# Kernel optimization log

Measured on AMD Instinct MI355X. Metric: run time of the kernel, lower is better.

Reference implementation:

```python
import jax, jax.numpy as jnp
import numpy as np

_EPS = 1e-8  # cosine-similarity clamp, matching F.cosine_similarity
_MAX_NODES = 50000


def _sig(x):
    return 1.0 / (1.0 + np.exp(-x))


def _build_structure(seqs, emb, comp_l, comp_r, cb, max_nodes=_MAX_NODES):
    """Host-side faithful replay of Banyan.compose()'s sequential greedy
    agglomerative merge. Returns the (data-dependent) merge schedule so the
    differentiable part can be replayed in jax. The similarity computation uses
    detached node values in the original, so the structure is a constant wrt
    differentiation. Dropout is run in eval mode (identity)."""
    E = emb.shape[1]
    sl, sr = _sig(comp_l), _sig(comp_r)  # (4,)
    uniq = np.unique(seqs)
    lookup = np.zeros(int(uniq.max()) + 1, dtype=np.int64)
    lookup[uniq] = np.arange(len(uniq))
    lookup[-1] = -1  # batch-max token is padding
    index = lookup[seqs]
    leaves = uniq[:-1]
    n_c = np.zeros((max_nodes, E), dtype=np.float32)
    n_c[: len(leaves)] = emb[leaves]
    t_c = np.full((max_nodes, 3), -1, dtype=np.int64)
    c_c = np.full((max_nodes, 2), -1, dtype=np.int64)
    md = int(index.max())
    B = index.shape[0]
    rows = np.arange(B)
    steps = []
    while index.shape[1] != 1:
        valid = index != -1  # -1 entries are always trailing
        W = index.shape[1]
        sims = np.zeros((B, W, E), dtype=np.float32)
        sims[valid] = n_c[index[valid]]
        a, b = sims[:, :-1], sims[:, 1:]
        na = np.maximum(np.linalg.norm(a, axis=2), _EPS)
        nb = np.maximum(np.linalg.norm(b, axis=2), _EPS)
        cos = (a * b).sum(2) / (na * nb)
        cos[~valid[:, 1:]] = -np.inf  # pairs whose right slot is empty
        max_sim = cos.argmax(1)  # (B,)
        retrieval = np.stack([max_sim, max_sim + 1], axis=1)  # (B, 2)
        completion = ~np.all(index[:, 1:] == -1, axis=1)
        r_c = retrieval[completion].reshape(-1)
        idx_c = index[completion]
        if idx_c.size:
            rt = np.repeat(np.arange(idx_c.shape[0]), 2)
            src = idx_c[rt, r_c].reshape(-1, 2)
            keep_src = ~((src[:, None, :] == c_c[None, :, :]).all(2)).any(1)
            src = np.unique(src[keep_src], axis=0)
            if src.size:
                k = src.shape[0]
                dst = md + 1 + np.arange(k)
                md = int(dst.max())
                l = n_c[src[:, 0]].reshape(k, 4, 4)
                r = n_c[src[:, 1]].reshape(k, 4, 4)
                n_c[dst] = (l * sl + r * sr + cb).reshape(k, E)
                c_c[dst] = src
                steps.append((src.copy(), dst.copy()))
                L, R = r_c[::2], r_c[1::2]
                l_t = np.concatenate([L, L - 1, R])
                r_n = R + 1
                r_n = np.where(r_n > idx_c.max(), -1, r_n)
                r_t = np.concatenate([R, L, r_n])
                t = np.concatenate([l_t, r_t]).reshape(-1, 3)
                t = np.unique(t, axis=0)
                keep_t = ~((t[:, None, :] == t_c[None, :, :]).all(2)).any(1)
                t = t[keep_t]
                adds = int((t_c != -1).all(1).sum())
                t_c[adds : adds + t.shape[0]] = t
        keep = np.ones(index.shape, dtype=bool)
        keep[rows[completion], max_sim[completion]] = False
        if (~completion).any():
            keep[~completion, -1] = False
        index = index[keep].reshape(B, -1)
    targets = t_c[(t_c != -1).all(1)]
    return leaves, steps, md, targets


def _replay(embedding, comp_l, comp_r, cb, leaves, steps, md, targets):
    """Differentiable replay of the recorded merge schedule + loss."""
    E = embedding.shape[1]
    sl = jax.nn.sigmoid(comp_l)
    sr = jax.nn.sigmoid(comp_r)

    def comp(l, r):  # LCCompose with 4 channels of width 4 (E = 16)
        return (l.reshape(-1, 4, 4) * sl + r.reshape(-1, 4, 4) * sr + cb).reshape(-1, E)

    n_c = jnp.zeros((md + 1, E), embedding.dtype)
    n_c = n_c.at[: leaves.shape[0]].set(embedding[leaves])
    for src, dst in steps:  # inherently sequential merge schedule
        n_c = n_c.at[dst].set(comp(n_c[src[:, 0]], n_c[src[:, 1]]))
    lefts = n_c[targets[:, 1]]
    rights = n_c[targets[:, 2]]
    logits = comp(lefts, rights) @ n_c.T  # [T, N], K=16 -> memory bound
    logp = jax.nn.log_softmax(logits, axis=-1)
    lbl = jnp.asarray(targets[:, 0])
    return -jnp.take_along_axis(logp, lbl[:, None], axis=1).mean()


def setup_inputs() -> dict:
    key = jax.random.key(0)
    ks = jax.random.split(key, 5)
    B, S, V, E = 48, 160, 32000, 16
    seqs = jax.random.randint(ks[0], (B, S), 0, V - 1)
    lens = jax.random.randint(ks[1], (B,), S // 2, S)  # at least 1 pad per row
    seqs = jnp.where(jnp.arange(S)[None, :] < lens[:, None], seqs, V - 1)
    embedding = jax.random.normal(ks[2], (V, E), jnp.float32)
    comp_l = jax.random.uniform(ks[3], (4,), jnp.float32, 0.6, 0.9)
    comp_r = jax.random.uniform(ks[4], (4,), jnp.float32, 0.6, 0.9)
    cb = jnp.zeros((4,), jnp.float32)
    return {"seqs": seqs, "embedding": embedding, "comp_l": comp_l, "comp_r": comp_r, "cb": cb}


def reference(seqs, embedding, comp_l, comp_r, cb):
    leaves, steps, md, targets = _build_structure(
        np.asarray(seqs), np.asarray(embedding), np.asarray(comp_l),
        np.asarray(comp_r), np.asarray(cb))
    return _replay(embedding, comp_l, comp_r, cb, leaves, steps, md, targets)
```

## Files before the change

### kernel.cpp

```cpp
#include <hip/hip_runtime.h>
#include <math.h>
#include <limits.h>

#define NT 1024
#define BB 48
#define SS 160
#define VV 32000
#define PADTOK 31999
#define EE 16
#define CAP 20000
#define NWRD 640
#define PHN 32768
#define TBW (1 << 19)

__device__ int      g_pres[32768];
__device__ int      g_rank[32768];
__device__ float    g_nc[CAP][EE];
__device__ float    g_nrm[CAP];
__device__ unsigned g_ph[PHN];
__device__ unsigned g_tbm[TBW];
__device__ unsigned g_tck[CAP];
__device__ int      g_tg[CAP][3];
__device__ float    g_lo[CAP];
__device__ int      g_T, g_N;
__device__ float    g_sl[4], g_sr[4], g_cb[4];

__device__ __forceinline__ unsigned vload(const unsigned* p) {
    return *(const volatile unsigned*)p;
}

__device__ __forceinline__ float np_sum16(const float* p) {
    float r0 = __fadd_rn(p[0], p[8]);
    float r1 = __fadd_rn(p[1], p[9]);
    float r2 = __fadd_rn(p[2], p[10]);
    float r3 = __fadd_rn(p[3], p[11]);
    float r4 = __fadd_rn(p[4], p[12]);
    float r5 = __fadd_rn(p[5], p[13]);
    float r6 = __fadd_rn(p[6], p[14]);
    float r7 = __fadd_rn(p[7], p[15]);
    float a = __fadd_rn(__fadd_rn(r0, r1), __fadd_rn(r2, r3));
    float b = __fadd_rn(__fadd_rn(r4, r5), __fadd_rn(r6, r7));
    return __fadd_rn(a, b);
}

__device__ __forceinline__ int key_valid(unsigned k) {
    return (((k >> 16) & 255u) != 0u) && (((k >> 8) & 255u) != 0u) && ((k & 255u) != 0u);
}

__global__ __launch_bounds__(256)
void init_kernel()
{
    int i = blockIdx.x * 256 + threadIdx.x;
    if (i < TBW)   g_tbm[i] = 0u;
    if (i < PHN)   g_ph[i] = 0xFFFFFFFFu;
    if (i < 32768) g_pres[i] = 0;
    if (i < CAP)   g_tck[i] = 0u;
}

__global__ __launch_bounds__(NT)
void build_kernel(const int* __restrict__ seqs, const float* __restrict__ emb,
                  const float* __restrict__ comp_l, const float* __restrict__ comp_r,
                  const float* __restrict__ cbp)
{
    const int tid  = threadIdx.x;
    const int lane = tid & 63;
    const int wv   = tid >> 6;

    __shared__ short    s_idx[BB][SS];
    __shared__ float    s_cos[BB][SS];
    __shared__ int      s_nv[BB], s_ms[BB], s_comp[BB], s_rowmax[BB];
    __shared__ unsigned s_pkey[BB];
    __shared__ int      s_L[BB], s_R[BB], s_found[BB];
    __shared__ unsigned s_skey[BB], s_ssorted[BB];
    __shared__ int      s_cA[BB], s_cB[BB], s_dst[BB];
    __shared__ unsigned s_tkey[2 * BB], s_tsorted[2 * BB], s_stk[2 * BB];
    __shared__ float    s_newcos[BB];
    __shared__ unsigned s_tvb[NWRD];
    __shared__ int s_ncand, s_kcnt, s_mx, s_adds;
    __shared__ int s_md, s_hwm, s_nleaves;
    __shared__ int s_scan[NT / 64];
    __shared__ float s_sl4[4], s_sr4[4], s_cb4[4];

    if (tid < NWRD) s_tvb[tid] = 0u;
    for (int i = tid; i < BB * SS; i += NT) g_pres[seqs[i]] = 1;
    __syncthreads();
    int base = tid * 32;
    int c = 0;
    for (int k = 0; k < 32; ++k) { int v = base + k; if (v < VV) c += g_pres[v]; }
    int incl = c;
    for (int off = 1; off < 64; off <<= 1) {
        int t = __shfl_up(incl, off);
        if (lane >= off) incl += t;
    }
    if (lane == 63) s_scan[wv] = incl;
    __syncthreads();
    if (tid == 0) {
        int run = 0;
        for (int w = 0; w < NT / 64; ++w) { int t = s_scan[w]; s_scan[w] = run; run += t; }
        s_nleaves = run - 1;
        s_md = run - 2;
        s_hwm = 0;
    }
    __syncthreads();
    {
        int run = s_scan[wv] + incl - c;
        for (int k = 0; k < 32; ++k) {
            int v = base + k;
            if (v < VV && g_pres[v]) g_rank[v] = run++;
        }
    }
    __syncthreads();
    for (int v = tid; v < VV; v += NT) {
        if (g_pres[v] && v != PADTOK) {
            int r = g_rank[v];
            #pragma unroll
            for (int e = 0; e < EE; ++e) g_nc[r][e] = emb[v * EE + e];
        }
    }
    if (tid < 4) {
        float sl = 1.0f / (1.0f + expf(-comp_l[tid]));
        float sr = 1.0f / (1.0f + expf(-comp_r[tid]));
        s_sl4[tid] = sl; s_sr4[tid] = sr; s_cb4[tid] = cbp[tid];
        g_sl[tid] = sl;  g_sr[tid] = sr;  g_cb[tid] = cbp[tid];
    }
    for (int i = tid; i < BB * SS; i += NT) {
        int tok = seqs[i];
        s_idx[i / SS][i % SS] = (short)((tok == PADTOK) ? -1 : g_rank[tok]);
    }
    __syncthreads();
    const int nleaves = s_nleaves;
    for (int l = tid; l < nleaves; l += NT) {
        float p[EE];
        #pragma unroll
        for (int e = 0; e < EE; ++e) { float x = g_nc[l][e]; p[e] = __fmul_rn(x, x); }
        g_nrm[l] = fmaxf(__fsqrt_rn(np_sum16(p)), 1e-8f);
    }
    if (tid < BB) {
        int cnt = 0;
        for (int p = 0; p < SS; ++p) cnt += (s_idx[tid][p] >= 0);
        s_nv[tid] = cnt;
    }
    __syncthreads();
    for (int i = tid; i < BB * (SS - 1); i += NT) {
        int r = i / (SS - 1), p = i % (SS - 1);
        if (p < s_nv[r] - 1) {
            int a = s_idx[r][p], b = s_idx[r][p + 1];
            const float* pa = g_nc[a];
            const float* pb = g_nc[b];
            float pr[EE];
            #pragma unroll
            for (int e = 0; e < EE; ++e) pr[e] = __fmul_rn(pa[e], pb[e]);
            s_cos[r][p] = __fdiv_rn(np_sum16(pr), __fmul_rn(g_nrm[a], g_nrm[b]));
        }
    }
    __syncthreads();

    for (int it = 0; it < SS - 1; ++it) {
        const int W = SS - it;

        for (int row = wv; row < BB; row += 16) {
            int nv = s_nv[row];
            int npairs = nv - 1;
            float best = -INFINITY; int bidx = INT_MAX;
            for (int p = lane; p < npairs; p += 64) {
                float cv = s_cos[row][p];
                if (cv > best) { best = cv; bidx = p; }
            }
            int rmax = INT_MIN;
            for (int p = lane; p < W; p += 64) { int v = (int)s_idx[row][p]; if (v > rmax) rmax = v; }
            for (int off = 32; off >= 1; off >>= 1) {
                float ob = __shfl_down(best, off);
                int   oi = __shfl_down(bidx, off);
                int   om = __shfl_down(rmax, off);
                if (ob > best || (ob == best && oi < bidx)) { best = ob; bidx = oi; }
                if (om > rmax) rmax = om;
            }
            if (lane == 0) {
                s_ms[row] = (bidx == INT_MAX) ? 0 : bidx;
                s_comp[row] = (nv > 1) ? 1 : 0;
                s_rowmax[row] = rmax;
            }
        }
        if (tid == 0) s_adds = 0;
        __syncthreads();

        if (wv == 0) {
            int flag = (lane < BB) ? s_comp[lane] : 0;
            unsigned long long m = __ballot(flag);
            int rm = flag ? s_rowmax[lane] : INT_MIN;
            if (flag) {
                int pos = __popcll(m & ((1ULL << lane) - 1ULL));
                int ms = s_ms[lane];
                int a = s_idx[lane][ms], b = s_idx[lane][ms + 1];
                s_pkey[pos] = ((unsigned)a << 16) | (unsigned)b;
                s_L[pos] = ms; s_R[pos] = ms + 1;
            }
            for (int off = 32; off >= 1; off >>= 1) { int o = __shfl_down(rm, off); if (o > rm) rm = o; }
            if (lane == 0) { s_ncand = __popcll(m); s_mx = rm; }
        } else if (wv <= 3) {
            int loc = 0;
            for (int w = tid - 64; w < NWRD; w += 192) loc += __popc(s_tvb[w]);
            for (int off = 32; off >= 1; off >>= 1) loc += __shfl_down(loc, off);
            if (lane == 0 && loc) atomicAdd(&s_adds, loc);
        } else {
            int i = tid - 256;
            int row = i >> 4, e = i & 15;
            if (s_comp[row] && s_ms[row] >= 1) {
                int a = (int)s_idx[row][s_ms[row] - 1];
                int b = (int)s_idx[row][s_ms[row] + 1];
                float p = __fmul_rn(g_nc[a][e], g_nc[b][e]);
                p = __fadd_rn(p, __shfl_xor(p, 8, 16));
                p = __fadd_rn(p, __shfl_xor(p, 1, 16));
                p = __fadd_rn(p, __shfl_xor(p, 2, 16));
                p = __fadd_rn(p, __shfl_xor(p, 4, 16));
                if (e == 0) s_newcos[row] = __fdiv_rn(p, __fmul_rn(g_nrm[a], g_nrm[b]));
            }
        }
        __syncthreads();

        const int ncand = s_ncand;
        if (wv == 0) {
            if (lane < ncand) {
                unsigned k = s_pkey[lane];
                unsigned h = (k * 2654435761u) >> 17;
                int found = 0;
                while (true) {
                    unsigned v = vload(&g_ph[h]);
                    if (v == k) { found = 1; break; }
                    if (v == 0xFFFFFFFFu) break;
                    h = (h + 1) & (PHN - 1);
                }
                s_found[lane] = found;
            }
        } else if (wv <= 2) {
            int j = tid - 64;
            if (j < 2 * ncand) {
                int comps[3];
                #pragma unroll
                for (int cc = 0; cc < 3; ++cc) {
                    int i = 3 * j + cc;
                    int seg = i / ncand, q = i - seg * ncand;
                    int v;
                    switch (seg) {
                        case 0: v = s_L[q]; break;
                        case 1: v = s_L[q] - 1; break;
                        case 2: v = s_R[q]; break;
                        case 3: v = s_R[q]; break;
                        case 4: v = s_L[q]; break;
                        default: { int rn = s_R[q] + 1; v = (rn > s_mx) ? -1 : rn; } break;
                    }
                    comps[cc] = v;
                }
                s_tkey[j] = ((unsigned)(comps[0] + 1) << 16) | ((unsigned)(comps[1] + 1) << 8)
                          | (unsigned)(comps[2] + 1);
            }
        }
        __syncthreads();

        if (wv == 0) {
            int flag = (lane < ncand) ? (s_found[lane] == 0) : 0;
            unsigned long long m = __ballot(flag);
            if (flag) {
                int pos = __popcll(m & ((1ULL << lane) - 1ULL));
                s_skey[pos] = s_pkey[lane];
            }
            int kn = __popcll(m);
            if (lane < kn) {
                unsigned ki = s_skey[lane];
                int rk = 0;
                for (int j = 0; j < kn; ++j) {
                    unsigned kj = s_skey[j];
                    if (kj < ki || (kj == ki && j < lane)) rk++;
                }
                s_ssorted[rk] = ki;
            }
            int mdold = s_md;
            int f2 = 0;
            if (lane < kn) {
                unsigned k = s_ssorted[lane];
                f2 = (lane == 0) || (k != s_ssorted[lane - 1]);
            }
            unsigned long long m2 = __ballot(f2);
            int kcnt = __popcll(m2);
            if (f2) {
                int pos = __popcll(m2 & ((1ULL << lane) - 1ULL));
                unsigned k = s_ssorted[lane];
                s_cA[pos] = (int)(k >> 16);
                s_cB[pos] = (int)(k & 0xFFFFu);
                s_dst[pos] = mdold + 1 + pos;
                unsigned h = (k * 2654435761u) >> 17;
                while (true) {
                    unsigned prev = atomicCAS(&g_ph[h], 0xFFFFFFFFu, k);
                    if (prev == 0xFFFFFFFFu) break;
                    h = (h + 1) & (PHN - 1);
                }
            }
            if (lane == 0) { s_kcnt = kcnt; s_md = mdold + kcnt; }
        } else if (wv <= 2) {
            int j = tid - 64;
            int mt0 = 2 * ncand;
            if (j < mt0) {
                unsigned ki = s_tkey[j];
                int rk = 0;
                for (int jj = 0; jj < mt0; ++jj) {
                    unsigned kj = s_tkey[jj];
                    if (kj < ki || (kj == ki && jj < j)) rk++;
                }
                s_tsorted[rk] = ki;
            }
        }
        __syncthreads();

        const int kcnt = s_kcnt;
        if (wv == 0) {
            if (kcnt > 0) {
                int mt0 = 2 * ncand;
                int cnt = 0;
                #pragma unroll
                for (int chunk = 0; chunk < 2; ++chunk) {
                    int e = chunk * 64 + lane;
                    int flag = 0;
                    if (e < mt0) {
                        unsigned k = s_tsorted[e];
                        flag = (e == 0) || (k != s_tsorted[e - 1]);
                    }
                    unsigned long long m = __ballot(flag);
                    if (flag) {
                        int pos = cnt + __popcll(m & ((1ULL << lane) - 1ULL));
                        s_stk[pos] = s_tsorted[e];
                    }
                    cnt += __popcll(m);
                }
                const int mt = cnt;
                int f0 = 0, f1 = 0;
                {
                    int j = lane;
                    if (j < mt) { unsigned k = s_stk[j]; f0 = (k == 0u) || ((vload(&g_tbm[k >> 5]) >> (k & 31)) & 1u); }
                }
                {
                    int j = 64 + lane;
                    if (j < mt) { unsigned k = s_stk[j]; f1 = (k == 0u) || ((vload(&g_tbm[k >> 5]) >> (k & 31)) & 1u); }
                }
                int adds = s_adds;
                int cnt2 = 0;
                #pragma unroll
                for (int chunk = 0; chunk < 2; ++chunk) {
                    int j = chunk * 64 + lane;
                    int f = chunk ? f1 : f0;
                    int flag = (j < mt) && !f;
                    unsigned long long m = __ballot(flag);
                    if (flag) {
                        int pos = adds + cnt2 + __popcll(m & ((1ULL << lane) - 1ULL));
                        unsigned k = s_stk[j];
                        unsigned old = g_tck[pos];
                        if (old) atomicAnd(&g_tbm[old >> 5], ~(1u << (old & 31)));
                        atomicOr(&g_tbm[k >> 5], 1u << (k & 31));
                        g_tck[pos] = k;
                        int w = pos >> 5; unsigned bm = 1u << (pos & 31);
                        atomicAnd(&s_tvb[w], ~bm);
                        if (key_valid(k)) atomicOr(&s_tvb[w], bm);
                    }
                    cnt2 += __popcll(m);
                }
                if (lane == 0) { int e2 = adds + cnt2; if (e2 > s_hwm) s_hwm = e2; }
            }
        } else if (wv <= 12) {
            for (int sub = 0; sub < 4; ++sub) {
                int row = (wv - 1) * 4 + sub;
                if (s_comp[row]) {
                    int ms = s_ms[row];
                    for (int p = ms + lane; p <= W - 2; p += 64) {
                        short v = s_idx[row][p + 1];
                        float cv = s_cos[row][p + 1];
                        s_idx[row][p] = v;
                        s_cos[row][p] = cv;
                    }
                    if (lane == 0) {
                        s_nv[row] -= 1;
                        if (ms >= 1) s_cos[row][ms - 1] = s_newcos[row];
                    }
                }
            }
        } else {
            for (int i = tid - 832; i < kcnt * EE; i += 192) {
                int j = i >> 4, e = i & 15;
                float lv = g_nc[s_cA[j]][e], rv = g_nc[s_cB[j]][e];
                g_nc[s_dst[j]][e] = lv * s_sl4[e & 3] + rv * s_sr4[e & 3] + s_cb4[e & 3];
            }
        }
        __syncthreads();
    }

    {
        int hw = s_hwm;
        int per = (hw + NT - 1) / NT;
        int b2 = tid * per;
        int cnt = 0;
        for (int k = 0; k < per; ++k) {
            int e = b2 + k;
            if (e < hw && key_valid(g_tck[e])) cnt++;
        }
        int incl2 = cnt;
        for (int off = 1; off < 64; off <<= 1) {
            int t = __shfl_up(incl2, off);
            if (lane >= off) incl2 += t;
        }
        if (lane == 63) s_scan[wv] = incl2;
        __syncthreads();
        if (tid == 0) {
            int run = 0;
            for (int w = 0; w < NT / 64; ++w) { int t = s_scan[w]; s_scan[w] = run; run += t; }
            g_T = run;
            g_N = s_md + 1;
        }
        __syncthreads();
        int off2 = s_scan[wv] + incl2 - cnt;
        for (int k = 0; k < per; ++k) {
            int e = b2 + k;
            if (e < hw) {
                unsigned kk = g_tck[e];
                if (key_valid(kk)) {
                    g_tg[off2][0] = (int)((kk >> 16) & 255u) - 1;
                    g_tg[off2][1] = (int)((kk >> 8) & 255u) - 1;
                    g_tg[off2][2] = (int)(kk & 255u) - 1;
                    off2++;
                }
            }
        }
    }
}

__global__ __launch_bounds__(256)
void loss_kernel()
{
    __shared__ float s_u[EE];
    __shared__ float s_m[256], s_s[256];
    __shared__ float s_xlab;
    const int tid = threadIdx.x;
    const int T = g_T, N = g_N;
    for (int ti = blockIdx.x; ti < T; ti += gridDim.x) {
        int lab = g_tg[ti][0], l = g_tg[ti][1], r = g_tg[ti][2];
        if (tid < EE)
            s_u[tid] = g_nc[l][tid] * g_sl[tid & 3] + g_nc[r][tid] * g_sr[tid & 3] + g_cb[tid & 3];
        __syncthreads();
        float u[EE];
        #pragma unroll
        for (int e = 0; e < EE; ++e) u[e] = s_u[e];
        float m = -INFINITY, s = 0.0f;
        for (int j = tid; j < N; j += 256) {
            const float* pj = g_nc[j];
            float x = 0.f;
            #pragma unroll
            for (int e = 0; e < EE; ++e) x += u[e] * pj[e];
            if (x > m) { s = s * expf(m - x) + 1.0f; m = x; }
            else s += expf(x - m);
            if (j == lab) s_xlab = x;
        }
        s_m[tid] = m; s_s[tid] = s;
        __syncthreads();
        for (int st = 128; st >= 1; st >>= 1) {
            if (tid < st) {
                float m1 = s_m[tid], s1 = s_s[tid];
                float m2 = s_m[tid + st], s2 = s_s[tid + st];
                if (m2 == -INFINITY) {  }
                else if (m2 > m1) { s1 = s1 * expf(m1 - m2) + s2; m1 = m2; }
                else { s1 = s1 + s2 * expf(m2 - m1); }
                s_m[tid] = m1; s_s[tid] = s1;
            }
            __syncthreads();
        }
        if (tid == 0) g_lo[ti] = s_m[0] + logf(s_s[0]) - s_xlab;
        __syncthreads();
    }
}

__global__ __launch_bounds__(256)
void finish_kernel(float* __restrict__ out)
{
    __shared__ float s_p[256];
    const int tid = threadIdx.x;
    const int T = g_T;
    float acc = 0.f;
    for (int i = tid; i < T; i += 256) acc += g_lo[i];
    s_p[tid] = acc;
    __syncthreads();
    for (int st = 128; st >= 1; st >>= 1) {
        if (tid < st) s_p[tid] += s_p[tid + st];
        __syncthreads();
    }
    if (tid == 0) out[0] = (T > 0) ? (s_p[0] / (float)T) : 0.0f;
}

extern "C" void kernel_launch(void* const* d_in, const int* in_sizes, int n_in,
                              void* d_out, int out_size, void* d_ws, size_t ws_size,
                              hipStream_t stream) {
    const int*   seqs = (const int*)d_in[0];
    const float* emb  = (const float*)d_in[1];
    const float* cl   = (const float*)d_in[2];
    const float* cr   = (const float*)d_in[3];
    const float* cb   = (const float*)d_in[4];
    float* out = (float*)d_out;
    init_kernel<<<dim3(2048), dim3(256), 0, stream>>>();
    build_kernel<<<dim3(1), dim3(NT), 0, stream>>>(seqs, emb, cl, cr, cb);
    loss_kernel<<<dim3(2048), dim3(256), 0, stream>>>();
    finish_kernel<<<dim3(1), dim3(256), 0, stream>>>(out);
}
```

Before: 1.614 ms.

## Split monolithic build into per-row merge, bookkeeping, compose, and tiled loss kernels

Replaces the single-block 1024-thread build kernel with a pipeline of kernels. Leaf copy and norms run grid-wide, and each row's greedy merge trajectory is computed independently by one 64-thread block. A single-wave bookkeeping kernel then replays the cross-row dedup and target generation from those trajectories, and composed node vectors are computed in a separate parallel kernel. The loss kernel is retiled to handle 8 targets per block with wave-shuffle reductions and fast exp/log intrinsics. This trades more launches and the approximate __expf/__logf for removing the serial per-iteration block-wide synchronisation.

```diff
diff --git a/kernel.cpp b/kernel.cpp
--- a/kernel.cpp
+++ b/kernel.cpp
@@ -2,14 +2,12 @@
 #include <math.h>
 #include <limits.h>
 
-#define NT 1024
 #define BB 48
 #define SS 160
 #define VV 32000
 #define PADTOK 31999
 #define EE 16
 #define CAP 20000
-#define NWRD 640
 #define PHN 32768
 #define TBW (1 << 19)
 
@@ -20,9 +18,12 @@
 __device__ unsigned g_ph[PHN];
 __device__ unsigned g_tbm[TBW];
 __device__ unsigned g_tck[CAP];
+__device__ unsigned long long g_traj[(SS - 1) * BB];
+__device__ int      g_steps[BB];
+__device__ unsigned long long g_new[CAP];
 __device__ int      g_tg[CAP][3];
 __device__ float    g_lo[CAP];
-__device__ int      g_T, g_N;
+__device__ int      g_T, g_N, g_nl, g_md0, g_hwm, g_mdfin, g_ncnt;
 __device__ float    g_sl[4], g_sr[4], g_cb[4];
 
 __device__ __forceinline__ unsigned vload(const unsigned* p) {
@@ -47,6 +48,29 @@
     return (((k >> 16) & 255u) != 0u) && (((k >> 8) & 255u) != 0u) && ((k & 255u) != 0u);
 }
 
+__device__ __forceinline__ unsigned make_tkey(int j, int ncand, int mx,
+                                              const int* sL, const int* sR) {
+    int comps[3];
+    #pragma unroll
+    for (int cc = 0; cc < 3; ++cc) {
+        int i = 3 * j + cc;
+        int seg = 0;
+        while (i >= ncand) { i -= ncand; ++seg; }
+        int v;
+        switch (seg) {
+            case 0: v = sL[i]; break;
+            case 1: v = sL[i] - 1; break;
+            case 2: v = sR[i]; break;
+            case 3: v = sR[i]; break;
+            case 4: v = sL[i]; break;
+            default: { int rn = sR[i] + 1; v = (rn > mx) ? -1 : rn; } break;
+        }
+        comps[cc] = v;
+    }
+    return ((unsigned)(comps[0] + 1) << 16) | ((unsigned)(comps[1] + 1) << 8)
+         | (unsigned)(comps[2] + 1);
+}
+
 __global__ __launch_bounds__(256)
 void init_kernel()
 {
@@ -57,35 +81,15 @@
     if (i < CAP)   g_tck[i] = 0u;
 }
 
-__global__ __launch_bounds__(NT)
-void build_kernel(const int* __restrict__ seqs, const float* __restrict__ emb,
-                  const float* __restrict__ comp_l, const float* __restrict__ comp_r,
-                  const float* __restrict__ cbp)
-{
-    const int tid  = threadIdx.x;
-    const int lane = tid & 63;
-    const int wv   = tid >> 6;
-
-    __shared__ short    s_idx[BB][SS];
-    __shared__ float    s_cos[BB][SS];
-    __shared__ int      s_nv[BB], s_ms[BB], s_comp[BB], s_rowmax[BB];
-    __shared__ unsigned s_pkey[BB];
-    __shared__ int      s_L[BB], s_R[BB], s_found[BB];
-    __shared__ unsigned s_skey[BB], s_ssorted[BB];
-    __shared__ int      s_cA[BB], s_cB[BB], s_dst[BB];
-    __shared__ unsigned s_tkey[2 * BB], s_tsorted[2 * BB], s_stk[2 * BB];
-    __shared__ float    s_newcos[BB];
-    __shared__ unsigned s_tvb[NWRD];
-    __shared__ int s_ncand, s_kcnt, s_mx, s_adds;
-    __shared__ int s_md, s_hwm, s_nleaves;
-    __shared__ int s_scan[NT / 64];
-    __shared__ float s_sl4[4], s_sr4[4], s_cb4[4];
-
-    if (tid < NWRD) s_tvb[tid] = 0u;
-    for (int i = tid; i < BB * SS; i += NT) g_pres[seqs[i]] = 1;
-    __syncthreads();
-    int base = tid * 32;
-    int c = 0;
+__global__ __launch_bounds__(1024)
+void rank_kernel(const int* __restrict__ seqs, const float* __restrict__ comp_l,
+                 const float* __restrict__ comp_r, const float* __restrict__ cbp)
+{
+    const int tid = threadIdx.x, lane = tid & 63, wv = tid >> 6;
+    __shared__ int s_scan[16];
+    for (int i = tid; i < BB * SS; i += 1024) g_pres[seqs[i]] = 1;
+    __syncthreads();
+    int base = tid * 32, c = 0;
     for (int k = 0; k < 32; ++k) { int v = base + k; if (v < VV) c += g_pres[v]; }
     int incl = c;
     for (int off = 1; off < 64; off <<= 1) {
@@ -96,380 +100,424 @@
     __syncthreads();
     if (tid == 0) {
         int run = 0;
-        for (int w = 0; w < NT / 64; ++w) { int t = s_scan[w]; s_scan[w] = run; run += t; }
-        s_nleaves = run - 1;
-        s_md = run - 2;
-        s_hwm = 0;
-    }
-    __syncthreads();
-    {
-        int run = s_scan[wv] + incl - c;
-        for (int k = 0; k < 32; ++k) {
-            int v = base + k;
-            if (v < VV && g_pres[v]) g_rank[v] = run++;
-        }
-    }
-    __syncthreads();
-    for (int v = tid; v < VV; v += NT) {
-        if (g_pres[v] && v != PADTOK) {
-            int r = g_rank[v];
-            #pragma unroll
-            for (int e = 0; e < EE; ++e) g_nc[r][e] = emb[v * EE + e];
-        }
+        for (int w = 0; w < 16; ++w) { int t = s_scan[w]; s_scan[w] = run; run += t; }
+        g_nl = run - 1;
+        g_md0 = run - 2;
+    }
+    __syncthreads();
+    int run = s_scan[wv] + incl - c;
+    for (int k = 0; k < 32; ++k) {
+        int v = base + k;
+        if (v < VV && g_pres[v]) g_rank[v] = run++;
     }
     if (tid < 4) {
         float sl = 1.0f / (1.0f + expf(-comp_l[tid]));
         float sr = 1.0f / (1.0f + expf(-comp_r[tid]));
-        s_sl4[tid] = sl; s_sr4[tid] = sr; s_cb4[tid] = cbp[tid];
-        g_sl[tid] = sl;  g_sr[tid] = sr;  g_cb[tid] = cbp[tid];
-    }
-    for (int i = tid; i < BB * SS; i += NT) {
-        int tok = seqs[i];
-        s_idx[i / SS][i % SS] = (short)((tok == PADTOK) ? -1 : g_rank[tok]);
-    }
-    __syncthreads();
-    const int nleaves = s_nleaves;
-    for (int l = tid; l < nleaves; l += NT) {
-        float p[EE];
-        #pragma unroll
-        for (int e = 0; e < EE; ++e) { float x = g_nc[l][e]; p[e] = __fmul_rn(x, x); }
-        g_nrm[l] = fmaxf(__fsqrt_rn(np_sum16(p)), 1e-8f);
-    }
-    if (tid < BB) {
+        g_sl[tid] = sl; g_sr[tid] = sr; g_cb[tid] = cbp[tid];
+    }
+}
+
+__global__ __launch_bounds__(256)
+void leaf_kernel(const float* __restrict__ emb)
+{
+    int v = blockIdx.x * 256 + threadIdx.x;
+    int stride = gridDim.x * 256;
+    for (; v < VV; v += stride) {
+        if (g_pres[v] && v != PADTOK) {
+            int r = g_rank[v];
+            float p[EE];
+            #pragma unroll
+            for (int e = 0; e < EE; ++e) {
+                float x = emb[v * EE + e];
+                g_nc[r][e] = x;
+                p[e] = __fmul_rn(x, x);
+            }
+            g_nrm[r] = fmaxf(__fsqrt_rn(np_sum16(p)), 1e-8f);
+        }
+    }
+}
+
+__global__ __launch_bounds__(64)
+void rowsim_kernel(const int* __restrict__ seqs)
+{
+    const int row = blockIdx.x;
+    const int lane = threadIdx.x;
+    __shared__ float s_vec[SS][17];
+    __shared__ float s_nrmp[SS];
+    __shared__ float s_cos[SS];
+    __shared__ int   s_id[SS];
+    __shared__ int   s_map[SS];
+    __shared__ int   s_nv0;
+
+    for (int p = lane; p < SS; p += 64) {
+        int tok = seqs[row * SS + p];
+        s_id[p] = (tok == PADTOK) ? -1 : g_rank[tok];
+        s_map[p] = p;
+    }
+    __syncthreads();
+    if (lane == 0) {
         int cnt = 0;
-        for (int p = 0; p < SS; ++p) cnt += (s_idx[tid][p] >= 0);
-        s_nv[tid] = cnt;
-    }
-    __syncthreads();
-    for (int i = tid; i < BB * (SS - 1); i += NT) {
-        int r = i / (SS - 1), p = i % (SS - 1);
-        if (p < s_nv[r] - 1) {
-            int a = s_idx[r][p], b = s_idx[r][p + 1];
-            const float* pa = g_nc[a];
-            const float* pb = g_nc[b];
-            float pr[EE];
+        for (int p = 0; p < SS; ++p) cnt += (s_id[p] >= 0);
+        s_nv0 = cnt;
+    }
+    __syncthreads();
+    const int nv0 = s_nv0;
+    #pragma unroll 4
+    for (int i = lane; i < nv0 * 4; i += 64) {
+        int p = i >> 2, q = i & 3;
+        const float4 v = ((const float4*)g_nc[s_id[p]])[q];
+        s_vec[p][q * 4 + 0] = v.x; s_vec[p][q * 4 + 1] = v.y;
+        s_vec[p][q * 4 + 2] = v.z; s_vec[p][q * 4 + 3] = v.w;
+    }
+    for (int p = lane; p < nv0; p += 64) s_nrmp[p] = g_nrm[s_id[p]];
+    __syncthreads();
+    for (int p = lane; p < nv0 - 1; p += 64) {
+        float pr[EE];
+        #pragma unroll
+        for (int e = 0; e < EE; ++e) pr[e] = __fmul_rn(s_vec[p][e], s_vec[p + 1][e]);
+        s_cos[p] = __fdiv_rn(np_sum16(pr), __fmul_rn(s_nrmp[p], s_nrmp[p + 1]));
+    }
+    __syncthreads();
+
+    int nv = nv0;
+    for (int st = 0; nv > 1; ++st, --nv) {
+        float best = -INFINITY; int bidx = INT_MAX; int rmax = INT_MIN;
+        for (int p = lane; p < nv; p += 64) {
+            int v = s_id[p];
+            if (v > rmax) rmax = v;
+            if (p < nv - 1) {
+                float cv = s_cos[p];
+                if (cv > best) { best = cv; bidx = p; }
+            }
+        }
+        #pragma unroll
+        for (int off = 32; off >= 1; off >>= 1) {
+            float ob = __shfl_xor(best, off);
+            int   oi = __shfl_xor(bidx, off);
+            int   om = __shfl_xor(rmax, off);
+            if (ob > best || (ob == best && oi < bidx)) { best = ob; bidx = oi; }
+            if (om > rmax) rmax = om;
+        }
+        const int ms = bidx;
+        if (lane == 0) {
+            unsigned long long a = (unsigned)s_id[ms];
+            unsigned long long b = (unsigned)s_id[ms + 1];
+            g_traj[st * BB + row] = (a << 48) | (b << 32)
+                                  | ((unsigned long long)(unsigned)ms << 16)
+                                  | (unsigned long long)(unsigned)rmax;
+        }
+        float ncv = 0.f;
+        if (ms >= 1 && lane < 16) {
+            int m1 = s_map[ms - 1], m2 = s_map[ms + 1];
+            float pp = __fmul_rn(s_vec[m1][lane], s_vec[m2][lane]);
+            pp = __fadd_rn(pp, __shfl_xor(pp, 8, 16));
+            pp = __fadd_rn(pp, __shfl_xor(pp, 1, 16));
+            pp = __fadd_rn(pp, __shfl_xor(pp, 2, 16));
+            pp = __fadd_rn(pp, __shfl_xor(pp, 4, 16));
+            ncv = __fdiv_rn(pp, __fmul_rn(s_nrmp[m1], s_nrmp[m2]));
+        }
+        __syncthreads();
+        int iv[3], mv[3]; float cv[3];
+        #pragma unroll
+        for (int k = 0; k < 3; ++k) {
+            int p = ms + lane + k * 64;
+            if (p < nv - 1) { iv[k] = s_id[p + 1]; mv[k] = s_map[p + 1]; cv[k] = s_cos[p + 1]; }
+        }
+        __syncthreads();
+        #pragma unroll
+        for (int k = 0; k < 3; ++k) {
+            int p = ms + lane + k * 64;
+            if (p < nv - 1) { s_id[p] = iv[k]; s_map[p] = mv[k]; s_cos[p] = cv[k]; }
+        }
+        if (ms >= 1 && lane == 0) s_cos[ms - 1] = ncv;
+        __syncthreads();
+    }
+    if (lane == 0) g_steps[row] = nv0 - 1;
+}
+
+__global__ __launch_bounds__(64)
+void book_kernel()
+{
+    const int lane = threadIdx.x;
+    __shared__ unsigned s_pk[64], s_ps[64];
+    __shared__ int s_Ld[64], s_Rd[64];
+    __shared__ unsigned s_tk[96], s_ts[96], s_stk[96];
+
+    const int steps = (lane < BB) ? g_steps[lane] : 0;
+    int md = g_md0;
+    int validcnt = 0, hwm = 0, ncnt = 0;
+
+    unsigned long long tr = (0 < steps) ? g_traj[lane] : 0ULL;
+    for (int it = 0; it < SS - 1; ++it) {
+        unsigned long long trn = ((it + 1) < steps) ? g_traj[(it + 1) * BB + lane] : 0ULL;
+        const int active = (it < steps) ? 1 : 0;
+        unsigned long long am = __ballot(active);
+        const int ncand = __popcll(am);
+        if (ncand > 0) {
+            const int adds = validcnt;
+            int a  = (int)(tr >> 48);
+            int b  = (int)((tr >> 32) & 0xFFFFULL);
+            int ms = (int)((tr >> 16) & 0xFFFFULL);
+            int mx = active ? (int)(tr & 0xFFFFULL) : INT_MIN;
             #pragma unroll
-            for (int e = 0; e < EE; ++e) pr[e] = __fmul_rn(pa[e], pb[e]);
-            s_cos[r][p] = __fdiv_rn(np_sum16(pr), __fmul_rn(g_nrm[a], g_nrm[b]));
-        }
-    }
-    __syncthreads();
-
-    for (int it = 0; it < SS - 1; ++it) {
-        const int W = SS - it;
-
-        for (int row = wv; row < BB; row += 16) {
-            int nv = s_nv[row];
-            int npairs = nv - 1;
-            float best = -INFINITY; int bidx = INT_MAX;
-            for (int p = lane; p < npairs; p += 64) {
-                float cv = s_cos[row][p];
-                if (cv > best) { best = cv; bidx = p; }
-            }
-            int rmax = INT_MIN;
-            for (int p = lane; p < W; p += 64) { int v = (int)s_idx[row][p]; if (v > rmax) rmax = v; }
             for (int off = 32; off >= 1; off >>= 1) {
-                float ob = __shfl_down(best, off);
-                int   oi = __shfl_down(bidx, off);
-                int   om = __shfl_down(rmax, off);
-                if (ob > best || (ob == best && oi < bidx)) { best = ob; bidx = oi; }
-                if (om > rmax) rmax = om;
-            }
-            if (lane == 0) {
-                s_ms[row] = (bidx == INT_MAX) ? 0 : bidx;
-                s_comp[row] = (nv > 1) ? 1 : 0;
-                s_rowmax[row] = rmax;
-            }
-        }
-        if (tid == 0) s_adds = 0;
-        __syncthreads();
-
-        if (wv == 0) {
-            int flag = (lane < BB) ? s_comp[lane] : 0;
-            unsigned long long m = __ballot(flag);
-            int rm = flag ? s_rowmax[lane] : INT_MIN;
-            if (flag) {
-                int pos = __popcll(m & ((1ULL << lane) - 1ULL));
-                int ms = s_ms[lane];
-                int a = s_idx[lane][ms], b = s_idx[lane][ms + 1];
-                s_pkey[pos] = ((unsigned)a << 16) | (unsigned)b;
-                s_L[pos] = ms; s_R[pos] = ms + 1;
-            }
-            for (int off = 32; off >= 1; off >>= 1) { int o = __shfl_down(rm, off); if (o > rm) rm = o; }
-            if (lane == 0) { s_ncand = __popcll(m); s_mx = rm; }
-        } else if (wv <= 3) {
-            int loc = 0;
-            for (int w = tid - 64; w < NWRD; w += 192) loc += __popc(s_tvb[w]);
-            for (int off = 32; off >= 1; off >>= 1) loc += __shfl_down(loc, off);
-            if (lane == 0 && loc) atomicAdd(&s_adds, loc);
-        } else {
-            int i = tid - 256;
-            int row = i >> 4, e = i & 15;
-            if (s_comp[row] && s_ms[row] >= 1) {
-                int a = (int)s_idx[row][s_ms[row] - 1];
-                int b = (int)s_idx[row][s_ms[row] + 1];
-                float p = __fmul_rn(g_nc[a][e], g_nc[b][e]);
-                p = __fadd_rn(p, __shfl_xor(p, 8, 16));
-                p = __fadd_rn(p, __shfl_xor(p, 1, 16));
-                p = __fadd_rn(p, __shfl_xor(p, 2, 16));
-                p = __fadd_rn(p, __shfl_xor(p, 4, 16));
-                if (e == 0) s_newcos[row] = __fdiv_rn(p, __fmul_rn(g_nrm[a], g_nrm[b]));
-            }
-        }
-        __syncthreads();
-
-        const int ncand = s_ncand;
-        if (wv == 0) {
+                int o = __shfl_xor(mx, off); if (o > mx) mx = o;
+            }
+            int cpos = __popcll(am & ((1ULL << lane) - 1ULL));
+            if (active) {
+                s_pk[cpos] = ((unsigned)a << 16) | (unsigned)b;
+                s_Ld[cpos] = ms; s_Rd[cpos] = ms + 1;
+            }
+            __syncthreads();
+            unsigned ki = (lane < ncand) ? s_pk[lane] : 0xFFFFFFFFu;
+            int rk = 0;
+            for (int j = 0; j < ncand; ++j) {
+                unsigned kj = s_pk[j];
+                if (kj < ki || (kj == ki && j < lane)) ++rk;
+            }
+            if (lane < ncand) s_ps[rk] = ki;
+            const int mt0 = 2 * ncand;
+            const int j1 = 64 + lane;
+            unsigned tk0 = 0xFFFFFFFFu, tk1 = 0xFFFFFFFFu;
+            if (lane < mt0) { tk0 = make_tkey(lane, ncand, mx, s_Ld, s_Rd); s_tk[lane] = tk0; }
+            if (j1 < mt0)   { tk1 = make_tkey(j1, ncand, mx, s_Ld, s_Rd);   s_tk[j1] = tk1; }
+            __syncthreads();
+            int r0 = 0, r1 = 0;
+            for (int j = 0; j < mt0; ++j) {
+                unsigned kj = s_tk[j];
+                if (kj < tk0 || (kj == tk0 && j < lane)) ++r0;
+                if (kj < tk1 || (kj == tk1 && j < j1)) ++r1;
+            }
+            if (lane < mt0) s_ts[r0] = tk0;
+            if (j1 < mt0)   s_ts[r1] = tk1;
+            __syncthreads();
+            unsigned k0 = s_ts[lane];
+            int fl0 = (lane < mt0) && (lane == 0 || k0 != s_ts[lane - 1]);
+            unsigned long long m0 = __ballot(fl0);
+            if (fl0) s_stk[__popcll(m0 & ((1ULL << lane) - 1ULL))] = k0;
+            int c0d = __popcll(m0);
+            unsigned k1 = (j1 < 96) ? s_ts[j1] : 0u;
+            int fl1 = (j1 < mt0) && (k1 != s_ts[j1 - 1]);
+            unsigned long long m1 = __ballot(fl1);
+            if (fl1) s_stk[c0d + __popcll(m1 & ((1ULL << lane) - 1ULL))] = k1;
+            const int mt = c0d + __popcll(m1);
+            __syncthreads();
+
+            unsigned psk = (lane < ncand) ? s_ps[lane] : 0u;
+            int pfound = 0;
             if (lane < ncand) {
-                unsigned k = s_pkey[lane];
-                unsigned h = (k * 2654435761u) >> 17;
-                int found = 0;
+                unsigned h = (psk * 2654435761u) >> 17;
                 while (true) {
                     unsigned v = vload(&g_ph[h]);
-                    if (v == k) { found = 1; break; }
+                    if (v == psk) { pfound = 1; break; }
                     if (v == 0xFFFFFFFFu) break;
                     h = (h + 1) & (PHN - 1);
                 }
-                s_found[lane] = found;
-            }
-        } else if (wv <= 2) {
-            int j = tid - 64;
-            if (j < 2 * ncand) {
-                int comps[3];
-                #pragma unroll
-                for (int cc = 0; cc < 3; ++cc) {
-                    int i = 3 * j + cc;
-                    int seg = i / ncand, q = i - seg * ncand;
-                    int v;
-                    switch (seg) {
-                        case 0: v = s_L[q]; break;
-                        case 1: v = s_L[q] - 1; break;
-                        case 2: v = s_R[q]; break;
-                        case 3: v = s_R[q]; break;
-                        case 4: v = s_L[q]; break;
-                        default: { int rn = s_R[q] + 1; v = (rn > s_mx) ? -1 : rn; } break;
-                    }
-                    comps[cc] = v;
-                }
-                s_tkey[j] = ((unsigned)(comps[0] + 1) << 16) | ((unsigned)(comps[1] + 1) << 8)
-                          | (unsigned)(comps[2] + 1);
-            }
-        }
-        __syncthreads();
-
-        if (wv == 0) {
-            int flag = (lane < ncand) ? (s_found[lane] == 0) : 0;
-            unsigned long long m = __ballot(flag);
-            if (flag) {
-                int pos = __popcll(m & ((1ULL << lane) - 1ULL));
-                s_skey[pos] = s_pkey[lane];
-            }
-            int kn = __popcll(m);
-            if (lane < kn) {
-                unsigned ki = s_skey[lane];
-                int rk = 0;
-                for (int j = 0; j < kn; ++j) {
-                    unsigned kj = s_skey[j];
-                    if (kj < ki || (kj == ki && j < lane)) rk++;
-                }
-                s_ssorted[rk] = ki;
-            }
-            int mdold = s_md;
-            int f2 = 0;
-            if (lane < kn) {
-                unsigned k = s_ssorted[lane];
-                f2 = (lane == 0) || (k != s_ssorted[lane - 1]);
-            }
-            unsigned long long m2 = __ballot(f2);
-            int kcnt = __popcll(m2);
-            if (f2) {
-                int pos = __popcll(m2 & ((1ULL << lane) - 1ULL));
-                unsigned k = s_ssorted[lane];
-                s_cA[pos] = (int)(k >> 16);
-                s_cB[pos] = (int)(k & 0xFFFFu);
-                s_dst[pos] = mdold + 1 + pos;
-                unsigned h = (k * 2654435761u) >> 17;
+            }
+            unsigned stk0 = (lane < mt) ? s_stk[lane] : 0u;
+            unsigned stk1 = (64 + lane < mt) ? s_stk[64 + lane] : 0u;
+            int tf0 = 1, tf1 = 1;
+            if (lane < mt)
+                tf0 = (stk0 == 0u) || ((vload(&g_tbm[stk0 >> 5]) >> (stk0 & 31)) & 1u);
+            if (64 + lane < mt)
+                tf1 = (stk1 == 0u) || ((vload(&g_tbm[stk1 >> 5]) >> (stk1 & 31)) & 1u);
+            unsigned old0 = vload(&g_tck[adds + lane]);
+            unsigned old1 = (lane < 32) ? vload(&g_tck[adds + 64 + lane]) : 0u;
+
+            int keptp = (lane < ncand) && !pfound;
+            int flp = keptp && (lane == 0 || s_ps[lane - 1] != psk);
+            unsigned long long mp = __ballot(flp);
+            int kcnt = __popcll(mp);
+            if (flp) {
+                int p3 = __popcll(mp & ((1ULL << lane) - 1ULL));
+                int dst = md + 1 + p3;
+                unsigned a2 = psk >> 16, b2 = psk & 0xFFFFu;
+                g_new[ncnt + p3] = ((unsigned long long)a2 << 42)
+                                 | ((unsigned long long)b2 << 21)
+                                 | (unsigned long long)(unsigned)dst;
+                unsigned h = (psk * 2654435761u) >> 17;
                 while (true) {
-                    unsigned prev = atomicCAS(&g_ph[h], 0xFFFFFFFFu, k);
+                    unsigned prev = atomicCAS(&g_ph[h], 0xFFFFFFFFu, psk);
                     if (prev == 0xFFFFFFFFu) break;
                     h = (h + 1) & (PHN - 1);
                 }
             }
-            if (lane == 0) { s_kcnt = kcnt; s_md = mdold + kcnt; }
-        } else if (wv <= 2) {
-            int j = tid - 64;
-            int mt0 = 2 * ncand;
-            if (j < mt0) {
-                unsigned ki = s_tkey[j];
-                int rk = 0;
-                for (int jj = 0; jj < mt0; ++jj) {
-                    unsigned kj = s_tkey[jj];
-                    if (kj < ki || (kj == ki && jj < j)) rk++;
+            md += kcnt; ncnt += kcnt;
+
+            if (kcnt > 0) {
+                int kept0 = (lane < mt) && !tf0;
+                int kept1 = (64 + lane < mt) && !tf1;
+                unsigned long long mk0 = __ballot(kept0);
+                int c0 = __popcll(mk0);
+                unsigned long long mk1 = __ballot(kept1);
+                int cnt2 = c0 + __popcll(mk1);
+                int q0 = __popcll(mk0 & ((1ULL << lane) - 1ULL));
+                int q1 = c0 + __popcll(mk1 & ((1ULL << lane) - 1ULL));
+                unsigned oldA = __shfl(old0, q0 & 63);
+                unsigned oB0 = __shfl(old0, q1 & 63);
+                unsigned oB1 = __shfl(old1, (q1 - 64) & 63);
+                unsigned oldB = (q1 < 64) ? oB0 : oB1;
+                int delta = 0;
+                if (kept0) {
+                    int pos = adds + q0;
+                    if (oldA) atomicAnd(&g_tbm[oldA >> 5], ~(1u << (oldA & 31)));
+                    atomicOr(&g_tbm[stk0 >> 5], 1u << (stk0 & 31));
+                    *(volatile unsigned*)&g_tck[pos] = stk0;
+                    delta += key_valid(stk0) - (oldA ? key_valid(oldA) : 0);
                 }
-                s_tsorted[rk] = ki;
-            }
-        }
-        __syncthreads();
-
-        const int kcnt = s_kcnt;
-        if (wv == 0) {
-            if (kcnt > 0) {
-                int mt0 = 2 * ncand;
-                int cnt = 0;
+                if (kept1) {
+                    int pos = adds + q1;
+                    if (oldB) atomicAnd(&g_tbm[oldB >> 5], ~(1u << (oldB & 31)));
+                    atomicOr(&g_tbm[stk1 >> 5], 1u << (stk1 & 31));
+                    *(volatile unsigned*)&g_tck[pos] = stk1;
+                    delta += key_valid(stk1) - (oldB ? key_valid(oldB) : 0);
+                }
                 #pragma unroll
-                for (int chunk = 0; chunk < 2; ++chunk) {
-                    int e = chunk * 64 + lane;
-                    int flag = 0;
-                    if (e < mt0) {
-                        unsigned k = s_tsorted[e];
-                        flag = (e == 0) || (k != s_tsorted[e - 1]);
-                    }
-                    unsigned long long m = __ballot(flag);
-                    if (flag) {
-                        int pos = cnt + __popcll(m & ((1ULL << lane) - 1ULL));
-                        s_stk[pos] = s_tsorted[e];
-                    }
-                    cnt += __popcll(m);
-                }
-                const int mt = cnt;
-                int f0 = 0, f1 = 0;
-                {
-                    int j = lane;
-                    if (j < mt) { unsigned k = s_stk[j]; f0 = (k == 0u) || ((vload(&g_tbm[k >> 5]) >> (k & 31)) & 1u); }
-                }
-                {
-                    int j = 64 + lane;
-                    if (j < mt) { unsigned k = s_stk[j]; f1 = (k == 0u) || ((vload(&g_tbm[k >> 5]) >> (k & 31)) & 1u); }
-                }
-                int adds = s_adds;
-                int cnt2 = 0;
-                #pragma unroll
-                for (int chunk = 0; chunk < 2; ++chunk) {
-                    int j = chunk * 64 + lane;
-                    int f = chunk ? f1 : f0;
-                    int flag = (j < mt) && !f;
-                    unsigned long long m = __ballot(flag);
-                    if (flag) {
-                        int pos = adds + cnt2 + __popcll(m & ((1ULL << lane) - 1ULL));
-                        unsigned k = s_stk[j];
-                        unsigned old = g_tck[pos];
-                        if (old) atomicAnd(&g_tbm[old >> 5], ~(1u << (old & 31)));
-                        atomicOr(&g_tbm[k >> 5], 1u << (k & 31));
-                        g_tck[pos] = k;
-                        int w = pos >> 5; unsigned bm = 1u << (pos & 31);
-                        atomicAnd(&s_tvb[w], ~bm);
-                        if (key_valid(k)) atomicOr(&s_tvb[w], bm);
-                    }
-                    cnt2 += __popcll(m);
-                }
-                if (lane == 0) { int e2 = adds + cnt2; if (e2 > s_hwm) s_hwm = e2; }
-            }
-        } else if (wv <= 12) {
-            for (int sub = 0; sub < 4; ++sub) {
-                int row = (wv - 1) * 4 + sub;
-                if (s_comp[row]) {
-                    int ms = s_ms[row];
-                    for (int p = ms + lane; p <= W - 2; p += 64) {
-                        short v = s_idx[row][p + 1];
-                        float cv = s_cos[row][p + 1];
-                        s_idx[row][p] = v;
-                        s_cos[row][p] = cv;
-                    }
-                    if (lane == 0) {
-                        s_nv[row] -= 1;
-                        if (ms >= 1) s_cos[row][ms - 1] = s_newcos[row];
-                    }
-                }
-            }
-        } else {
-            for (int i = tid - 832; i < kcnt * EE; i += 192) {
-                int j = i >> 4, e = i & 15;
-                float lv = g_nc[s_cA[j]][e], rv = g_nc[s_cB[j]][e];
-                g_nc[s_dst[j]][e] = lv * s_sl4[e & 3] + rv * s_sr4[e & 3] + s_cb4[e & 3];
-            }
-        }
-        __syncthreads();
-    }
-
-    {
-        int hw = s_hwm;
-        int per = (hw + NT - 1) / NT;
-        int b2 = tid * per;
-        int cnt = 0;
-        for (int k = 0; k < per; ++k) {
-            int e = b2 + k;
-            if (e < hw && key_valid(g_tck[e])) cnt++;
-        }
-        int incl2 = cnt;
-        for (int off = 1; off < 64; off <<= 1) {
-            int t = __shfl_up(incl2, off);
-            if (lane >= off) incl2 += t;
-        }
-        if (lane == 63) s_scan[wv] = incl2;
-        __syncthreads();
-        if (tid == 0) {
-            int run = 0;
-            for (int w = 0; w < NT / 64; ++w) { int t = s_scan[w]; s_scan[w] = run; run += t; }
-            g_T = run;
-            g_N = s_md + 1;
-        }
-        __syncthreads();
-        int off2 = s_scan[wv] + incl2 - cnt;
-        for (int k = 0; k < per; ++k) {
-            int e = b2 + k;
-            if (e < hw) {
-                unsigned kk = g_tck[e];
-                if (key_valid(kk)) {
-                    g_tg[off2][0] = (int)((kk >> 16) & 255u) - 1;
-                    g_tg[off2][1] = (int)((kk >> 8) & 255u) - 1;
-                    g_tg[off2][2] = (int)(kk & 255u) - 1;
-                    off2++;
-                }
-            }
-        }
+                for (int off = 32; off >= 1; off >>= 1) delta += __shfl_xor(delta, off);
+                validcnt += delta;
+                int e2 = adds + cnt2;
+                if (e2 > hwm) hwm = e2;
+            }
+        }
+        tr = trn;
+    }
+    if (lane == 0) { g_hwm = hwm; g_mdfin = md; g_ncnt = ncnt; }
+}
+
+__global__ __launch_bounds__(1024)
+void final_kernel()
+{
+    const int tid = threadIdx.x, lane = tid & 63, wv = tid >> 6;
+    __shared__ int s_scan[16];
+    const int hw = g_hwm;
+    int per = (hw + 1023) / 1024;
+    int b2 = tid * per;
+    int cnt = 0;
+    for (int k = 0; k < per; ++k) {
+        int e = b2 + k;
+        if (e < hw && key_valid(g_tck[e])) cnt++;
+    }
+    int incl = cnt;
+    for (int off = 1; off < 64; off <<= 1) {
+        int t = __shfl_up(incl, off);
+        if (lane >= off) incl += t;
+    }
+    if (lane == 63) s_scan[wv] = incl;
+    __syncthreads();
+    if (tid == 0) {
+        int run = 0;
+        for (int w = 0; w < 16; ++w) { int t = s_scan[w]; s_scan[w] = run; run += t; }
+        g_T = run;
+        g_N = g_mdfin + 1;
+    }
+    __syncthreads();
+    int off2 = s_scan[wv] + incl - cnt;
+    for (int k = 0; k < per; ++k) {
+        int e = b2 + k;
+        if (e < hw) {
+            unsigned kk = g_tck[e];
+            if (key_valid(kk)) {
+                g_tg[off2][0] = (int)((kk >> 16) & 255u) - 1;
+                g_tg[off2][1] = (int)((kk >> 8) & 255u) - 1;
+                g_tg[off2][2] = (int)(kk & 255u) - 1;
+                off2++;
+            }
+        }
+    }
+}
+
+__global__ __launch_bounds__(256)
+void compose_kernel()
+{
+    int n16 = g_ncnt * EE;
+    int i = blockIdx.x * 256 + threadIdx.x;
+    int stride = gridDim.x * 256;
+    for (; i < n16; i += stride) {
+        int j = i >> 4, e = i & 15;
+        unsigned long long v = g_new[j];
+        int dst = (int)(v & 0x1FFFFFULL);
+        int b = (int)((v >> 21) & 0x1FFFFFULL);
+        int a = (int)(v >> 42);
+        g_nc[dst][e] = g_nc[a][e] * g_sl[e & 3] + g_nc[b][e] * g_sr[e & 3] + g_cb[e & 3];
     }
 }
 
 __global__ __launch_bounds__(256)
 void loss_kernel()
 {
-    __shared__ float s_u[EE];
-    __shared__ float s_m[256], s_s[256];
-    __shared__ float s_xlab;
     const int tid = threadIdx.x;
     const int T = g_T, N = g_N;
-    for (int ti = blockIdx.x; ti < T; ti += gridDim.x) {
-        int lab = g_tg[ti][0], l = g_tg[ti][1], r = g_tg[ti][2];
-        if (tid < EE)
-            s_u[tid] = g_nc[l][tid] * g_sl[tid & 3] + g_nc[r][tid] * g_sr[tid & 3] + g_cb[tid & 3];
-        __syncthreads();
-        float u[EE];
-        #pragma unroll
-        for (int e = 0; e < EE; ++e) u[e] = s_u[e];
-        float m = -INFINITY, s = 0.0f;
+    __shared__ float s_u[8][17];
+    __shared__ int   s_lab[8];
+    __shared__ float s_pm[4][8], s_ps2[4][8], s_px[4][8];
+    const int wv2 = tid >> 6, ln2 = tid & 63;
+    int ntile = (T + 7) >> 3;
+    for (int tile = blockIdx.x; tile < ntile; tile += gridDim.x) {
+        int t0 = tile * 8;
+        if (tid < 128) {
+            int t = t0 + (tid >> 4), e = tid & 15;
+            int tt = (t < T) ? t : 0;
+            int l = g_tg[tt][1], r = g_tg[tt][2];
+            s_u[tid >> 4][e] = g_nc[l][e] * g_sl[e & 3] + g_nc[r][e] * g_sr[e & 3] + g_cb[e & 3];
+        } else if (tid < 136) {
+            int t = t0 + tid - 128;
+            s_lab[tid - 128] = (t < T) ? g_tg[t][0] : -1;
+        }
+        __syncthreads();
+        float u[128];
+        #pragma unroll
+        for (int t = 0; t < 8; ++t)
+            #pragma unroll
+            for (int e = 0; e < 16; ++e) u[t * 16 + e] = s_u[t][e];
+        int lab[8];
+        #pragma unroll
+        for (int t = 0; t < 8; ++t) lab[t] = s_lab[t];
+        float m[8], s[8], xl[8];
+        #pragma unroll
+        for (int t = 0; t < 8; ++t) { m[t] = -INFINITY; s[t] = 0.f; xl[t] = 0.f; }
         for (int j = tid; j < N; j += 256) {
-            const float* pj = g_nc[j];
-            float x = 0.f;
+            const float4* pj = (const float4*)g_nc[j];
+            float4 v0 = pj[0], v1 = pj[1], v2 = pj[2], v3 = pj[3];
+            float vec[16] = {v0.x, v0.y, v0.z, v0.w, v1.x, v1.y, v1.z, v1.w,
+                             v2.x, v2.y, v2.z, v2.w, v3.x, v3.y, v3.z, v3.w};
             #pragma unroll
-            for (int e = 0; e < EE; ++e) x += u[e] * pj[e];
-            if (x > m) { s = s * expf(m - x) + 1.0f; m = x; }
-            else s += expf(x - m);
-            if (j == lab) s_xlab = x;
-        }
-        s_m[tid] = m; s_s[tid] = s;
-        __syncthreads();
-        for (int st = 128; st >= 1; st >>= 1) {
-            if (tid < st) {
-                float m1 = s_m[tid], s1 = s_s[tid];
-                float m2 = s_m[tid + st], s2 = s_s[tid + st];
-                if (m2 == -INFINITY) {  }
-                else if (m2 > m1) { s1 = s1 * expf(m1 - m2) + s2; m1 = m2; }
-                else { s1 = s1 + s2 * expf(m2 - m1); }
-                s_m[tid] = m1; s_s[tid] = s1;
-            }
-            __syncthreads();
-        }
-        if (tid == 0) g_lo[ti] = s_m[0] + logf(s_s[0]) - s_xlab;
+            for (int t = 0; t < 8; ++t) {
+                float x = 0.f;
+                #pragma unroll
+                for (int e = 0; e < 16; ++e) x = fmaf(vec[e], u[t * 16 + e], x);
+                if (x > m[t]) { s[t] = s[t] * __expf(m[t] - x) + 1.0f; m[t] = x; }
+                else s[t] += __expf(x - m[t]);
+                if (j == lab[t]) xl[t] = x;
+            }
+        }
+        #pragma unroll
+        for (int t = 0; t < 8; ++t) {
+            float mm = m[t], ss = s[t], xx = xl[t];
+            #pragma unroll
+            for (int off = 32; off >= 1; off >>= 1) {
+                float om = __shfl_xor(mm, off);
+                float os = __shfl_xor(ss, off);
+                xx += __shfl_xor(xx, off);
+                if (om == -INFINITY) { }
+                else if (om > mm) { ss = ss * __expf(mm - om) + os; mm = om; }
+                else ss = ss + os * __expf(om - mm);
+            }
+            if (ln2 == 0) { s_pm[wv2][t] = mm; s_ps2[wv2][t] = ss; s_px[wv2][t] = xx; }
+        }
+        __syncthreads();
+        if (tid < 8) {
+            float mm = s_pm[0][tid], ss = s_ps2[0][tid], xx = s_px[0][tid];
+            #pragma unroll
+            for (int w = 1; w < 4; ++w) {
+                float om = s_pm[w][tid], os = s_ps2[w][tid];
+                xx += s_px[w][tid];
+                if (om == -INFINITY) { }
+                else if (om > mm) { ss = ss * __expf(mm - om) + os; mm = om; }
+                else ss = ss + os * __expf(om - mm);
+            }
+            int t = t0 + tid;
+            if (t < T) g_lo[t] = mm + __logf(ss) - xx;
+        }
         __syncthreads();
     }
 }
@@ -501,7 +549,12 @@
     const float* cb   = (const float*)d_in[4];
     float* out = (float*)d_out;
     init_kernel<<<dim3(2048), dim3(256), 0, stream>>>();
-    build_kernel<<<dim3(1), dim3(NT), 0, stream>>>(seqs, emb, cl, cr, cb);
-    loss_kernel<<<dim3(2048), dim3(256), 0, stream>>>();
+    rank_kernel<<<dim3(1), dim3(1024), 0, stream>>>(seqs, cl, cr, cb);
+    leaf_kernel<<<dim3(128), dim3(256), 0, stream>>>(emb);
+    rowsim_kernel<<<dim3(BB), dim3(64), 0, stream>>>(seqs);
+    book_kernel<<<dim3(1), dim3(64), 0, stream>>>();
+    final_kernel<<<dim3(1), dim3(1024), 0, stream>>>();
+    compose_kernel<<<dim3(128), dim3(256), 0, stream>>>();
+    loss_kernel<<<dim3(1024), dim3(256), 0, stream>>>();
     finish_kernel<<<dim3(1), dim3(256), 0, stream>>>(out);
 }
```

Result: slower. 1.756 ms (+8.8%).
